# Kernel optimization log

Hardware: AMD Instinct MI355X
Metric: run time of the kernel (lower is better)

Reference implementation:

```python
import jax, jax.numpy as jnp
import numpy as np

K = 9          # kernel taps along the space-filling curve
SIGMA = 1.0    # gaussian bandwidth (conv2 uses SIGMA * stride, stride=1)
EPS = 1e-5     # BatchNorm eps


def _weighted_conv(x, w, coords, indices, reindices, sigma):
    """Gather points into curve order, run a k-tap 1D conv whose taps are
    modulated by a Gaussian of coordinate distance, scatter back.
    x: [B,C,N], w: [O,C,K], coords: [B,3,N], indices/reindices: [B,N]."""
    B, C, N = x.shape
    pad = K // 2
    idx = indices[:, None, :]
    xp = jnp.take_along_axis(x, jnp.broadcast_to(idx, (B, C, N)), axis=2)        # curve order
    cp = jnp.take_along_axis(coords, jnp.broadcast_to(idx, (B, 3, N)), axis=2)
    x_pad = jnp.pad(xp, ((0, 0), (0, 0), (pad, pad)))
    c_pad = jnp.pad(cp, ((0, 0), (0, 0), (pad, pad)))
    inv_s2 = 1.0 / (sigma * sigma)
    out = jnp.zeros((B, w.shape[0], N), x.dtype)
    for t in range(K):  # small fixed loop over kernel taps
        xw = x_pad[:, :, t:t + N]                     # [B,C,N]
        rel = c_pad[:, :, t:t + N] - cp               # [B,3,N]
        g = jnp.exp(-jnp.sum(rel * rel, axis=1) * inv_s2)  # [B,N] gaussian weight
        out = out + jnp.einsum('oc,bcn->bon', w[:, :, t], xw * g[:, None, :])
    ridx = reindices[:, None, :]
    return jnp.take_along_axis(out, jnp.broadcast_to(ridx, out.shape), axis=2)


def _batchnorm1d(x, gamma, beta):
    # training-mode BN over (batch, points) per channel, biased variance
    mean = jnp.mean(x, axis=(0, 2), keepdims=True)
    var = jnp.mean((x - mean) ** 2, axis=(0, 2), keepdims=True)
    return gamma[None, :, None] * (x - mean) * jax.lax.rsqrt(var + EPS) + beta[None, :, None]


def setup_inputs() -> dict:
    key = jax.random.key(0)
    ks = jax.random.split(key, 6)
    B, C, N = 4, 128, 65536
    x = jax.random.normal(ks[0], (B, C, N), jnp.float32)
    coords = jax.random.uniform(ks[1], (B, 3, N), jnp.float32)
    perm = jnp.stack([jax.random.permutation(jax.random.fold_in(ks[2], b), N) for b in range(B)])
    indices = perm.astype(jnp.int32)
    reindices = jnp.argsort(perm, axis=1).astype(jnp.int32)
    w1 = jax.random.normal(ks[3], (C, C, K), jnp.float32) * 0.05
    w2 = jax.random.normal(ks[4], (C, C, K), jnp.float32) * 0.05
    gamma1 = jnp.ones((C,), jnp.float32)
    beta1 = jnp.zeros((C,), jnp.float32)
    gamma2 = jnp.ones((C,), jnp.float32)
    beta2 = jnp.zeros((C,), jnp.float32)
    return {"x": x, "coords": coords, "indices": indices, "reindices": reindices,
            "w1": w1, "gamma1": gamma1, "beta1": beta1,
            "w2": w2, "gamma2": gamma2, "beta2": beta2}


def reference(x, coords, indices, reindices, w1, gamma1, beta1, w2, gamma2, beta2):
    identity = x
    out = _weighted_conv(x, w1, coords, indices, reindices, SIGMA)
    out = jax.nn.relu(_batchnorm1d(out, gamma1, beta1))
    out = _weighted_conv(out, w2, coords, indices, reindices, SIGMA * 1)  # stride=1
    out = _batchnorm1d(out, gamma2, beta2)
    return jax.nn.relu(out + identity)
```

## Files before the change

kernel.cpp:

```cpp
#include <hip/hip_runtime.h>

#define Bn 4
#define Cn 128
#define Nn 65536
#define KT 9
#define T_OUT 256
#define T_HALO 264
#define XROW 136
#define GROW 264
#define FT 66

typedef _Float16 f16x8 __attribute__((ext_vector_type(8)));
typedef _Float16 f16x4 __attribute__((ext_vector_type(4)));
typedef float f32x4 __attribute__((ext_vector_type(4)));
typedef float f32x2 __attribute__((ext_vector_type(2)));

__global__ __launch_bounds__(256) void repack_w(const float* __restrict__ w1,
                                                const float* __restrict__ w2,
                                                _Float16* __restrict__ Wr) {
  int i = blockIdx.x * 256 + threadIdx.x;
  int c = i & 127;
  int o = (i >> 7) & 127;
  int t = (i >> 14) % KT;
  int cv = i / (KT << 14);
  const float* w = cv ? w2 : w1;
  Wr[i] = (_Float16)w[(o * 128 + c) * KT + t];
}

__global__ __launch_bounds__(256) void gather_x(const float* __restrict__ x,
                                                const int* __restrict__ reidx,
                                                _Float16* __restrict__ xp) {
  __shared__ float ft[128 * FT];
  int tid = threadIdx.x;
  int b = blockIdx.x >> 10;
  int n0 = (blockIdx.x & 1023) * 64;
  const float* xb = x + (size_t)b * Cn * Nn;
  {
    int cc = tid >> 4;
    int j4 = (tid & 15) * 4;
#pragma unroll
    for (int pass = 0; pass < 8; ++pass) {
      int c = pass * 16 + cc;
      f32x4 v = *(const f32x4*)(&xb[(size_t)c * Nn + n0 + j4]);
      *(f32x2*)(&ft[c * FT + j4]) = f32x2{v.x, v.y};
      *(f32x2*)(&ft[c * FT + j4 + 2]) = f32x2{v.z, v.w};
    }
  }
  __syncthreads();
  int ch = tid & 15;
  int rr = tid >> 4;
#pragma unroll
  for (int pass = 0; pass < 4; ++pass) {
    int r = pass * 16 + rr;
    int m = reidx[(size_t)b * Nn + n0 + r];
    f16x8 v;
#pragma unroll
    for (int k = 0; k < 8; ++k) v[k] = (_Float16)ft[(ch * 8 + k) * FT + r];
    *(f16x8*)(xp + ((size_t)b * Nn + m) * Cn + ch * 8) = v;
  }
}

__global__ __launch_bounds__(256) void gather_g(const float* __restrict__ coords,
                                                const int* __restrict__ indices,
                                                float* __restrict__ G) {
  __shared__ float cx[264], cy[264], cz[264];
  int tid = threadIdx.x;
  int b = blockIdx.x >> 8;
  int n0 = (blockIdx.x & 255) * 256;
  const float* cb = coords + (size_t)b * 3 * Nn;
  for (int i = tid; i < 264; i += 256) {
    int q = n0 - 4 + i;
    q = q < 0 ? 0 : (q > Nn - 1 ? Nn - 1 : q);
    int idx = indices[(size_t)b * Nn + q];
    cx[i] = cb[idx];
    cy[i] = cb[Nn + idx];
    cz[i] = cb[2 * Nn + idx];
  }
  __syncthreads();
  int m = n0 + tid;
  float x0 = cx[tid + 4], y0 = cy[tid + 4], z0 = cz[tid + 4];
  float* Gb = G + (size_t)b * KT * Nn;
#pragma unroll
  for (int t = 0; t < KT; ++t) {
    float dx = cx[tid + t] - x0;
    float dy = cy[tid + t] - y0;
    float dz = cz[tid + t] - z0;
    Gb[(size_t)t * Nn + m] = __expf(-(dx * dx + dy * dy + dz * dz));
  }
}

__global__ void bncoeff(const float* __restrict__ sums,
                        const float* __restrict__ gamma,
                        const float* __restrict__ beta,
                        float* __restrict__ coeff) {
  int c = threadIdx.x;
  const float inv = 1.0f / (float)((size_t)Bn * Nn);
  float mean = sums[c] * inv;
  float var = sums[128 + c] * inv - mean * mean;
  float a = gamma[c] * rsqrtf(var + 1e-5f);
  coeff[c] = a;
  coeff[128 + c] = beta[c] - mean * a;
}

__device__ __forceinline__ f16x8 scale8(f16x8 v, _Float16 g) {
  f16x8 r;
#pragma unroll
  for (int i = 0; i < 8; ++i) r[i] = v[i] * g;
  return r;
}

template <int TRANS>
__global__ __launch_bounds__(512) void conv_wlds(
    const _Float16* __restrict__ Xin, const _Float16* __restrict__ W,
    const float* __restrict__ G, _Float16* __restrict__ Yout,
    float* __restrict__ sums, const float* __restrict__ coeff) {
  __shared__ __align__(16) _Float16 Xs[T_HALO * XROW];
  __shared__ __align__(16) _Float16 Wlds[2][128 * XROW];
  __shared__ __align__(16) unsigned char aux[KT * GROW * 2];
  _Float16* Gs = (_Float16*)aux;
  float* red = (float*)aux;

  const int tid = threadIdx.x;
  const int b = blockIdx.x >> 8;
  const int p0 = (blockIdx.x & 255) * T_OUT;
  const int ch = tid & 15;

  f16x8 w0r[4], w1r[4];
#pragma unroll
  for (int i = 0; i < 4; ++i) {
    int q = i * 512 + tid;
    w0r[i] = *(const f16x8*)(W + (q >> 4) * 128 + (q & 15) * 8);
    w1r[i] = *(const f16x8*)(W + 16384 + (q >> 4) * 128 + (q & 15) * 8);
  }

#pragma unroll
  for (int pass = 0; pass < 9; ++pass) {
    int r = pass * 32 + (tid >> 4);
    if (r < T_HALO) {
      int q = p0 - 4 + r;
      f16x8 v = {0, 0, 0, 0, 0, 0, 0, 0};
      if (q >= 0 && q < Nn) {
        v = *(const f16x8*)(Xin + ((size_t)b * Nn + q) * Cn + ch * 8);
        if (TRANS) {
#pragma unroll
          for (int i = 0; i < 8; ++i) {
            float f = fmaxf(coeff[ch * 8 + i] * (float)v[i] + coeff[128 + ch * 8 + i], 0.f);
            v[i] = (_Float16)f;
          }
        }
      }
      *(f16x8*)(&Xs[r * XROW + ch * 8]) = v;
    }
  }
  {
    const float* gb = G + (size_t)b * KT * Nn + p0;
    for (int i = tid; i < KT * 256; i += 512) {
      int t = i >> 8;
      int p = i & 255;
      Gs[t * GROW + p] = (_Float16)gb[(size_t)t * Nn + p];
    }
  }
#pragma unroll
  for (int i = 0; i < 4; ++i) {
    int q = i * 512 + tid;
    *(f16x8*)(&Wlds[0][(q >> 4) * XROW + (q & 15) * 8]) = w0r[i];
    *(f16x8*)(&Wlds[1][(q >> 4) * XROW + (q & 15) * 8]) = w1r[i];
  }

  const int w = tid >> 6;
  const int lane = tid & 63;
  const int l15 = lane & 15;
  const int quad = lane >> 4;
  const int wm = w >> 1;
  const int wn = w & 1;

  f32x4 acc[2][8];
  const f32x4 z4 = {0.f, 0.f, 0.f, 0.f};
#pragma unroll
  for (int mt = 0; mt < 2; ++mt)
#pragma unroll
    for (int nt = 0; nt < 8; ++nt) acc[mt][nt] = z4;

  __syncthreads();

  f16x8 wpre[4];
#pragma unroll 1
  for (int t = 0; t < KT; ++t) {
    if (t <= KT - 3) {
      const _Float16* Wt2 = W + ((size_t)(t + 2) << 14);
#pragma unroll
      for (int i = 0; i < 4; ++i) {
        int q = i * 512 + tid;
        wpre[i] = *(const f16x8*)(Wt2 + (q >> 4) * 128 + (q & 15) * 8);
      }
    }

    _Float16 gt[8];
#pragma unroll
    for (int nt = 0; nt < 8; ++nt)
      gt[nt] = Gs[t * GROW + wn * 128 + nt * 16 + l15];

    const _Float16* Wb = &Wlds[t & 1][0];
#pragma unroll
    for (int ko = 0; ko < 4; ++ko) {
      f16x8 a2[2];
#pragma unroll
      for (int mt = 0; mt < 2; ++mt)
        a2[mt] = *(const f16x8*)(Wb + (wm * 32 + mt * 16 + l15) * XROW + ko * 32 + quad * 8);
#pragma unroll
      for (int nt = 0; nt < 8; ++nt) {
        f16x8 bv = *(const f16x8*)(&Xs[(wn * 128 + nt * 16 + l15 + t) * XROW + ko * 32 + quad * 8]);
        bv = scale8(bv, gt[nt]);
#pragma unroll
        for (int mt = 0; mt < 2; ++mt)
          acc[mt][nt] = __builtin_amdgcn_mfma_f32_16x16x32_f16(a2[mt], bv, acc[mt][nt], 0, 0, 0);
      }
    }

    __syncthreads();
    if (t <= KT - 3) {
#pragma unroll
      for (int i = 0; i < 4; ++i) {
        int q = i * 512 + tid;
        *(f16x8*)(&Wlds[t & 1][(q >> 4) * XROW + (q & 15) * 8]) = wpre[i];
      }
    }
  }

  f32x4 s4[2], q4[2];
#pragma unroll
  for (int mt = 0; mt < 2; ++mt) {
#pragma unroll
    for (int rg = 0; rg < 4; ++rg) {
      float s = 0.f, q = 0.f;
#pragma unroll
      for (int nt = 0; nt < 8; ++nt) {
        float v = acc[mt][nt][rg];
        s += v;
        q += v * v;
      }
#pragma unroll
      for (int m = 1; m < 16; m <<= 1) {
        s += __shfl_xor(s, m);
        q += __shfl_xor(q, m);
      }
      s4[mt][rg] = s;
      q4[mt][rg] = q;
    }
  }
  if (l15 == 0) {
#pragma unroll
    for (int mt = 0; mt < 2; ++mt) {
      int cbase = wm * 32 + mt * 16 + quad * 4;
      *(f32x4*)(&red[wn * 128 + cbase]) = s4[mt];
      *(f32x4*)(&red[256 + wn * 128 + cbase]) = q4[mt];
    }
  }

  _Float16* Os = Xs;
#pragma unroll
  for (int mt = 0; mt < 2; ++mt)
#pragma unroll
    for (int nt = 0; nt < 8; ++nt) {
      f16x4 o4;
#pragma unroll
      for (int rg = 0; rg < 4; ++rg) o4[rg] = (_Float16)acc[mt][nt][rg];
      *(f16x4*)(&Os[(wn * 128 + nt * 16 + l15) * XROW + wm * 32 + mt * 16 + quad * 4]) = o4;
    }
  __syncthreads();

  if (tid < 128) {
    atomicAdd(&sums[tid], red[tid] + red[128 + tid]);
    atomicAdd(&sums[128 + tid], red[256 + tid] + red[384 + tid]);
  }
#pragma unroll
  for (int pass = 0; pass < 8; ++pass) {
    int r = pass * 32 + (tid >> 4);
    f16x8 v = *(const f16x8*)(&Os[r * XROW + ch * 8]);
    *(f16x8*)(Yout + ((size_t)b * Nn + p0 + r) * Cn + ch * 8) = v;
  }
}

__global__ __launch_bounds__(256) void final_k(const _Float16* __restrict__ y2,
                                               const float* __restrict__ x,
                                               const int* __restrict__ reidx,
                                               const float* __restrict__ coeff,
                                               float* __restrict__ out) {
  __shared__ float ft[128 * FT];
  int tid = threadIdx.x;
  int b = blockIdx.x >> 10;
  int n0 = (blockIdx.x & 1023) * 64;
  {
    int ch = tid & 15;
#pragma unroll
    for (int pass = 0; pass < 4; ++pass) {
      int r = pass * 16 + (tid >> 4);
      int m = reidx[(size_t)b * Nn + n0 + r];
      f16x8 v = *(const f16x8*)(y2 + ((size_t)b * Nn + m) * Cn + ch * 8);
#pragma unroll
      for (int k = 0; k < 8; ++k) ft[(ch * 8 + k) * FT + r] = (float)v[k];
    }
  }
  __syncthreads();
  int cc = tid >> 4;
  int j4 = (tid & 15) * 4;
#pragma unroll
  for (int pass = 0; pass < 8; ++pass) {
    int c = pass * 16 + cc;
    float a = coeff[c];
    float bb = coeff[128 + c];
    f32x2 v0 = *(const f32x2*)(&ft[c * FT + j4]);
    f32x2 v1 = *(const f32x2*)(&ft[c * FT + j4 + 2]);
    size_t gi = ((size_t)b * Cn + c) * Nn + n0 + j4;
    f32x4 xv = *(const f32x4*)(&x[gi]);
    f32x4 r;
    r.x = fmaxf(a * v0.x + bb + xv.x, 0.f);
    r.y = fmaxf(a * v0.y + bb + xv.y, 0.f);
    r.z = fmaxf(a * v1.x + bb + xv.z, 0.f);
    r.w = fmaxf(a * v1.y + bb + xv.w, 0.f);
    *(f32x4*)(&out[gi]) = r;
  }
}

extern "C" void kernel_launch(void* const* d_in, const int* in_sizes, int n_in,
                              void* d_out, int out_size, void* d_ws, size_t ws_size,
                              hipStream_t stream) {
  (void)in_sizes; (void)n_in; (void)out_size; (void)ws_size;
  const float* x = (const float*)d_in[0];
  const float* coords = (const float*)d_in[1];
  const int* indices = (const int*)d_in[2];
  const int* reindices = (const int*)d_in[3];
  const float* w1 = (const float*)d_in[4];
  const float* gamma1 = (const float*)d_in[5];
  const float* beta1 = (const float*)d_in[6];
  const float* w2 = (const float*)d_in[7];
  const float* gamma2 = (const float*)d_in[8];
  const float* beta2 = (const float*)d_in[9];
  float* out = (float*)d_out;

  char* ws = (char*)d_ws;
  const size_t BUF0 = (size_t)Bn * Nn * Cn * sizeof(_Float16);
  _Float16* buf0 = (_Float16*)ws;
  float* sums1 = (float*)(ws + BUF0);
  float* sums2 = sums1 + 256;
  float* coeff1 = sums1 + 512;
  float* coeff2 = sums1 + 768;
  _Float16* Wr = (_Float16*)(ws + BUF0 + 4096);

  char* dob = (char*)d_out;
  _Float16* y1 = (_Float16*)dob;
  float* G = (float*)(dob + BUF0);

  hipMemsetAsync(sums1, 0, 512 * sizeof(float), stream);

  repack_w<<<1152, 256, 0, stream>>>(w1, w2, Wr);
  gather_x<<<Bn * 1024, 256, 0, stream>>>(x, reindices, buf0);
  gather_g<<<Bn * 256, 256, 0, stream>>>(coords, indices, G);

  conv_wlds<0><<<Bn * 256, 512, 0, stream>>>(buf0, Wr, G, y1, sums1, nullptr);
  bncoeff<<<1, 128, 0, stream>>>(sums1, gamma1, beta1, coeff1);
  conv_wlds<1><<<Bn * 256, 512, 0, stream>>>(y1, Wr + (size_t)KT * Cn * Cn, G,
                                             buf0, sums2, coeff1);
  bncoeff<<<1, 128, 0, stream>>>(sums2, gamma2, beta2, coeff2);
  final_k<<<Bn * 1024, 256, 0, stream>>>(buf0, x, reindices, coeff2, out);
}
```

Baseline: 524.2 us.

## Pre-swizzle weights into MFMA fragment order and retile waves to 2x4

Weights are repacked so each lane's A fragment is contiguous, and they are stored in LDS without row padding, so loads become linear 16-byte reads with no bank conflicts. The wave tiling changes from 4x2 (32 out-channels by 128 points) to 2x4 (64 out-channels by 64 points). Each wave now loads 4 A fragments and 4 scaled B fragments per k-step instead of 2 and 8, which reduces the per-element scaling of X fragments. The reduction scratch buffer grows to hold four partial sums per channel, and it must still fit inside the aux buffer.

```diff
diff --git a/kernel.cpp b/kernel.cpp
--- a/kernel.cpp
+++ b/kernel.cpp
@@ -19,10 +19,15 @@
                                                 const float* __restrict__ w2,
                                                 _Float16* __restrict__ Wr) {
   int i = blockIdx.x * 256 + threadIdx.x;
-  int c = i & 127;
-  int o = (i >> 7) & 127;
+  int j = i & 7;
+  int lane = (i >> 3) & 63;
+  int mt = (i >> 9) & 3;
+  int ko = (i >> 11) & 3;
+  int wm = (i >> 13) & 1;
   int t = (i >> 14) % KT;
   int cv = i / (KT << 14);
+  int o = wm * 64 + mt * 16 + (lane & 15);
+  int c = ko * 32 + (lane >> 4) * 8 + j;
   const float* w = cv ? w2 : w1;
   Wr[i] = (_Float16)w[(o * 128 + c) * KT + t];
 }
@@ -115,7 +120,7 @@
     const float* __restrict__ G, _Float16* __restrict__ Yout,
     float* __restrict__ sums, const float* __restrict__ coeff) {
   __shared__ __align__(16) _Float16 Xs[T_HALO * XROW];
-  __shared__ __align__(16) _Float16 Wlds[2][128 * XROW];
+  __shared__ __align__(16) _Float16 Wlds[2][16384];
   __shared__ __align__(16) unsigned char aux[KT * GROW * 2];
   _Float16* Gs = (_Float16*)aux;
   float* red = (float*)aux;
@@ -129,8 +134,8 @@
 #pragma unroll
   for (int i = 0; i < 4; ++i) {
     int q = i * 512 + tid;
-    w0r[i] = *(const f16x8*)(W + (q >> 4) * 128 + (q & 15) * 8);
-    w1r[i] = *(const f16x8*)(W + 16384 + (q >> 4) * 128 + (q & 15) * 8);
+    w0r[i] = *(const f16x8*)(W + q * 8);
+    w1r[i] = *(const f16x8*)(W + 16384 + q * 8);
   }
 
 #pragma unroll
@@ -163,23 +168,23 @@
 #pragma unroll
   for (int i = 0; i < 4; ++i) {
     int q = i * 512 + tid;
-    *(f16x8*)(&Wlds[0][(q >> 4) * XROW + (q & 15) * 8]) = w0r[i];
-    *(f16x8*)(&Wlds[1][(q >> 4) * XROW + (q & 15) * 8]) = w1r[i];
+    *(f16x8*)(&Wlds[0][q * 8]) = w0r[i];
+    *(f16x8*)(&Wlds[1][q * 8]) = w1r[i];
   }
 
   const int w = tid >> 6;
   const int lane = tid & 63;
   const int l15 = lane & 15;
   const int quad = lane >> 4;
-  const int wm = w >> 1;
-  const int wn = w & 1;
-
-  f32x4 acc[2][8];
+  const int wm = w >> 2;
+  const int wn = w & 3;
+
+  f32x4 acc[4][4];
   const f32x4 z4 = {0.f, 0.f, 0.f, 0.f};
 #pragma unroll
-  for (int mt = 0; mt < 2; ++mt)
-#pragma unroll
-    for (int nt = 0; nt < 8; ++nt) acc[mt][nt] = z4;
+  for (int mt = 0; mt < 4; ++mt)
+#pragma unroll
+    for (int nt = 0; nt < 4; ++nt) acc[mt][nt] = z4;
 
   __syncthreads();
 
@@ -191,29 +196,29 @@
 #pragma unroll
       for (int i = 0; i < 4; ++i) {
         int q = i * 512 + tid;
-        wpre[i] = *(const f16x8*)(Wt2 + (q >> 4) * 128 + (q & 15) * 8);
-      }
-    }
-
-    _Float16 gt[8];
-#pragma unroll
-    for (int nt = 0; nt < 8; ++nt)
-      gt[nt] = Gs[t * GROW + wn * 128 + nt * 16 + l15];
-
-    const _Float16* Wb = &Wlds[t & 1][0];
+        wpre[i] = *(const f16x8*)(Wt2 + q * 8);
+      }
+    }
+
+    _Float16 gt[4];
+#pragma unroll
+    for (int nt = 0; nt < 4; ++nt)
+      gt[nt] = Gs[t * GROW + wn * 64 + nt * 16 + l15];
+
+    const _Float16* Wb = &Wlds[t & 1][wm * 8192];
 #pragma unroll
     for (int ko = 0; ko < 4; ++ko) {
-      f16x8 a2[2];
-#pragma unroll
-      for (int mt = 0; mt < 2; ++mt)
-        a2[mt] = *(const f16x8*)(Wb + (wm * 32 + mt * 16 + l15) * XROW + ko * 32 + quad * 8);
-#pragma unroll
-      for (int nt = 0; nt < 8; ++nt) {
-        f16x8 bv = *(const f16x8*)(&Xs[(wn * 128 + nt * 16 + l15 + t) * XROW + ko * 32 + quad * 8]);
+      f16x8 a4[4];
+#pragma unroll
+      for (int mt = 0; mt < 4; ++mt)
+        a4[mt] = *(const f16x8*)(Wb + ko * 2048 + mt * 512 + lane * 8);
+#pragma unroll
+      for (int nt = 0; nt < 4; ++nt) {
+        f16x8 bv = *(const f16x8*)(&Xs[(wn * 64 + nt * 16 + l15 + t) * XROW + ko * 32 + quad * 8]);
         bv = scale8(bv, gt[nt]);
 #pragma unroll
-        for (int mt = 0; mt < 2; ++mt)
-          acc[mt][nt] = __builtin_amdgcn_mfma_f32_16x16x32_f16(a2[mt], bv, acc[mt][nt], 0, 0, 0);
+        for (int mt = 0; mt < 4; ++mt)
+          acc[mt][nt] = __builtin_amdgcn_mfma_f32_16x16x32_f16(a4[mt], bv, acc[mt][nt], 0, 0, 0);
       }
     }
 
@@ -222,19 +227,19 @@
 #pragma unroll
       for (int i = 0; i < 4; ++i) {
         int q = i * 512 + tid;
-        *(f16x8*)(&Wlds[t & 1][(q >> 4) * XROW + (q & 15) * 8]) = wpre[i];
-      }
-    }
-  }
-
-  f32x4 s4[2], q4[2];
-#pragma unroll
-  for (int mt = 0; mt < 2; ++mt) {
+        *(f16x8*)(&Wlds[t & 1][q * 8]) = wpre[i];
+      }
+    }
+  }
+
+  f32x4 s4[4], q4[4];
+#pragma unroll
+  for (int mt = 0; mt < 4; ++mt) {
 #pragma unroll
     for (int rg = 0; rg < 4; ++rg) {
       float s = 0.f, q = 0.f;
 #pragma unroll
-      for (int nt = 0; nt < 8; ++nt) {
+      for (int nt = 0; nt < 4; ++nt) {
         float v = acc[mt][nt][rg];
         s += v;
         q += v * v;
@@ -250,28 +255,30 @@
   }
   if (l15 == 0) {
 #pragma unroll
-    for (int mt = 0; mt < 2; ++mt) {
-      int cbase = wm * 32 + mt * 16 + quad * 4;
+    for (int mt = 0; mt < 4; ++mt) {
+      int cbase = wm * 64 + mt * 16 + quad * 4;
       *(f32x4*)(&red[wn * 128 + cbase]) = s4[mt];
-      *(f32x4*)(&red[256 + wn * 128 + cbase]) = q4[mt];
+      *(f32x4*)(&red[512 + wn * 128 + cbase]) = q4[mt];
     }
   }
 
   _Float16* Os = Xs;
 #pragma unroll
-  for (int mt = 0; mt < 2; ++mt)
-#pragma unroll
-    for (int nt = 0; nt < 8; ++nt) {
+  for (int mt = 0; mt < 4; ++mt)
+#pragma unroll
+    for (int nt = 0; nt < 4; ++nt) {
       f16x4 o4;
 #pragma unroll
       for (int rg = 0; rg < 4; ++rg) o4[rg] = (_Float16)acc[mt][nt][rg];
-      *(f16x4*)(&Os[(wn * 128 + nt * 16 + l15) * XROW + wm * 32 + mt * 16 + quad * 4]) = o4;
+      *(f16x4*)(&Os[(wn * 64 + nt * 16 + l15) * XROW + wm * 64 + mt * 16 + quad * 4]) = o4;
     }
   __syncthreads();
 
   if (tid < 128) {
-    atomicAdd(&sums[tid], red[tid] + red[128 + tid]);
-    atomicAdd(&sums[128 + tid], red[256 + tid] + red[384 + tid]);
+    atomicAdd(&sums[tid],
+              red[tid] + red[128 + tid] + red[256 + tid] + red[384 + tid]);
+    atomicAdd(&sums[128 + tid],
+              red[512 + tid] + red[640 + tid] + red[768 + tid] + red[896 + tid]);
   }
 #pragma unroll
   for (int pass = 0; pass < 8; ++pass) {
```

Result: no change. 517.8 us (-1.2%).
